# Performance work log

Measured on AMD Instinct MI355X. Metric: run time of the kernel, lower is better.

The kernel has to match this reference:

```python
import jax, jax.numpy as jnp
import numpy as np

A4 = 0.1
EPS = 1e-8  # torch.cosine_similarity eps


def setup_inputs() -> dict:
    key = jax.random.key(0)
    ks = jax.random.split(key, 7)
    N, D, C = 200000, 256, 7
    return {
        "seq": jax.random.normal(ks[0], (N, D), jnp.float32),
        "seq1": jax.random.normal(ks[1], (N, D), jnp.float32),
        "prompt": jax.random.normal(ks[2], (3, D), jnp.float32),
        "w_np": jnp.array([[0.5, 0.4, 0.3]], jnp.float32),  # weighted_prompt init
        "w_ds": jax.random.normal(ks[4], (1, D), jnp.float32) * 0.05,  # downstreamprompt weight
        "w_df": jnp.array([[0.0, 1.0]], jnp.float32),  # weighted_feature init
        "ave": jax.random.normal(ks[6], (C, D), jnp.float32),  # class prototypes (train=0)
    }


def reference(seq, seq1, prompt, w_np, w_ds, w_df, ave):
    # weighted_prompt -> ELU -> 1 + .
    weight = 1.0 + jax.nn.elu(w_np @ prompt)          # [1, D]
    rawret1 = weight * seq                             # [N, D]
    rawret2 = w_ds * seq                               # downstreamprompt
    rawret3 = jax.nn.elu(w_df[0, 0] * rawret1 + w_df[0, 1] * rawret2)
    rawret = rawret3 + A4 * seq1                       # [N, D]
    # per-row cosine similarity vs each class prototype, then softmax
    dots = rawret @ ave.T                              # [N, C]
    nr = jnp.linalg.norm(rawret, axis=1, keepdims=True)   # [N, 1]
    na = jnp.linalg.norm(ave, axis=1)                     # [C]
    sims = dots / jnp.maximum(nr * na[None, :], EPS)
    return jax.nn.softmax(sims, axis=1)
```

## Files before the change

### kernel.cpp

```cpp
#include <hip/hip_runtime.h>
#include <math.h>


__device__ __forceinline__ float elu1(float x) {
    return x > 0.0f ? x : __expf(x) - 1.0f;
}

__device__ __forceinline__ float wave_sum(float v) {
#pragma unroll
    for (int off = 32; off > 0; off >>= 1)
        v += __shfl_xor(v, off, 64);
    return v;
}

__global__ __launch_bounds__(256) void downprompt_kernel(
    const float* __restrict__ seq,
    const float* __restrict__ seq1,
    const float* __restrict__ prompt,
    const float* __restrict__ w_np,
    const float* __restrict__ w_ds,
    const float* __restrict__ w_df,
    const float* __restrict__ ave,
    float* __restrict__ out,
    int N)
{
    const int lane = threadIdx.x & 63;
    const int wavesPerBlock = blockDim.x >> 6;
    const int gwave = blockIdx.x * wavesPerBlock + (threadIdx.x >> 6);
    const int nwave = gridDim.x * wavesPerBlock;
    const int d0 = lane << 2;

    const float a  = w_df[0];
    const float b  = w_df[1];
    const float w0 = w_np[0], w1 = w_np[1], w2 = w_np[2];

    const float4 p0 = *(const float4*)(prompt +   0 + d0);
    const float4 p1 = *(const float4*)(prompt + 256 + d0);
    const float4 p2 = *(const float4*)(prompt + 512 + d0);
    const float4 wd = *(const float4*)(w_ds + d0);

    float coef[4];
    coef[0] = a * (1.0f + elu1(w0*p0.x + w1*p1.x + w2*p2.x)) + b * wd.x;
    coef[1] = a * (1.0f + elu1(w0*p0.y + w1*p1.y + w2*p2.y)) + b * wd.y;
    coef[2] = a * (1.0f + elu1(w0*p0.z + w1*p1.z + w2*p2.z)) + b * wd.z;
    coef[3] = a * (1.0f + elu1(w0*p0.w + w1*p1.w + w2*p2.w)) + b * wd.w;

    float av[7][4];
    float na[7];
#pragma unroll
    for (int c = 0; c < 7; ++c) {
        const float4 v = *(const float4*)(ave + c * 256 + d0);
        av[c][0] = v.x; av[c][1] = v.y; av[c][2] = v.z; av[c][3] = v.w;
        const float p = v.x*v.x + v.y*v.y + v.z*v.z + v.w*v.w;
        na[c] = sqrtf(wave_sum(p));
    }

    for (int row = gwave; row < N; row += nwave) {
        const float4 s = *(const float4*)(seq  + (size_t)row * 256 + d0);
        const float4 t = *(const float4*)(seq1 + (size_t)row * 256 + d0);

        float r[4];
        r[0] = elu1(coef[0] * s.x) + 0.1f * t.x;
        r[1] = elu1(coef[1] * s.y) + 0.1f * t.y;
        r[2] = elu1(coef[2] * s.z) + 0.1f * t.z;
        r[3] = elu1(coef[3] * s.w) + 0.1f * t.w;

        float acc[8];
#pragma unroll
        for (int c = 0; c < 7; ++c)
            acc[c] = r[0]*av[c][0] + r[1]*av[c][1] + r[2]*av[c][2] + r[3]*av[c][3];
        acc[7] = r[0]*r[0] + r[1]*r[1] + r[2]*r[2] + r[3]*r[3];

#pragma unroll
        for (int off = 32; off > 0; off >>= 1) {
#pragma unroll
            for (int k = 0; k < 8; ++k)
                acc[k] += __shfl_xor(acc[k], off, 64);
        }

        const float nr = sqrtf(acc[7]);
        float sims[7];
        float m = -INFINITY;
#pragma unroll
        for (int c = 0; c < 7; ++c) {
            const float den = fmaxf(nr * na[c], 1e-8f);
            sims[c] = acc[c] * __builtin_amdgcn_rcpf(den);
            m = fmaxf(m, sims[c]);
        }
        float sum = 0.0f, mye = 0.0f;
#pragma unroll
        for (int c = 0; c < 7; ++c) {
            const float e = __expf(sims[c] - m);
            sum += e;
            if (lane == c) mye = e;
        }
        if (lane < 7)
            out[(size_t)row * 7 + lane] = mye * __builtin_amdgcn_rcpf(sum);
    }
}

extern "C" void kernel_launch(void* const* d_in, const int* in_sizes, int n_in,
                              void* d_out, int out_size, void* d_ws, size_t ws_size,
                              hipStream_t stream) {
    const float* seq    = (const float*)d_in[0];
    const float* seq1   = (const float*)d_in[1];
    const float* prompt = (const float*)d_in[2];
    const float* w_np   = (const float*)d_in[3];
    const float* w_ds   = (const float*)d_in[4];
    const float* w_df   = (const float*)d_in[5];
    const float* ave    = (const float*)d_in[6];
    float* out = (float*)d_out;

    const int N = in_sizes[0] / 256;

    downprompt_kernel<<<2048, 256, 0, stream>>>(seq, seq1, prompt, w_np, w_ds,
                                                w_df, ave, out, N);
}
```

Measured before the change: 438.3 us.

## Map eight rows per wave with 8-lane groups and short shuffle reductions

```diff
diff --git a/kernel.cpp b/kernel.cpp
--- a/kernel.cpp
+++ b/kernel.cpp
@@ -2,15 +2,10 @@
 #include <math.h>
 
 
+#define NCLS 7
+
 __device__ __forceinline__ float elu1(float x) {
     return x > 0.0f ? x : __expf(x) - 1.0f;
-}
-
-__device__ __forceinline__ float wave_sum(float v) {
-#pragma unroll
-    for (int off = 32; off > 0; off >>= 1)
-        v += __shfl_xor(v, off, 64);
-    return v;
 }
 
 __global__ __launch_bounds__(256) void downprompt_kernel(
@@ -24,78 +19,95 @@
     float* __restrict__ out,
     int N)
 {
-    const int lane = threadIdx.x & 63;
-    const int wavesPerBlock = blockDim.x >> 6;
-    const int gwave = blockIdx.x * wavesPerBlock + (threadIdx.x >> 6);
-    const int nwave = gridDim.x * wavesPerBlock;
-    const int d0 = lane << 2;
+    __shared__ float s_coef[256];
+    __shared__ float s_rna[NCLS];
 
-    const float a  = w_df[0];
-    const float b  = w_df[1];
-    const float w0 = w_np[0], w1 = w_np[1], w2 = w_np[2];
+    const int tid = threadIdx.x;
 
-    const float4 p0 = *(const float4*)(prompt +   0 + d0);
-    const float4 p1 = *(const float4*)(prompt + 256 + d0);
-    const float4 p2 = *(const float4*)(prompt + 512 + d0);
-    const float4 wd = *(const float4*)(w_ds + d0);
+    {
+        const float a  = w_df[0], b = w_df[1];
+        const float w0 = w_np[0], w1 = w_np[1], w2 = w_np[2];
+        const float pd = w0 * prompt[tid] + w1 * prompt[256 + tid]
+                       + w2 * prompt[512 + tid];
+        s_coef[tid] = a * (1.0f + elu1(pd)) + b * w_ds[tid];
+    }
+    if (tid < NCLS) {
+        const float4* av4 = (const float4*)(ave + tid * 256);
+        float s = 0.0f;
+#pragma unroll
+        for (int i = 0; i < 64; ++i) {
+            const float4 v = av4[i];
+            s += v.x * v.x + v.y * v.y + v.z * v.z + v.w * v.w;
+        }
+        s_rna[tid] = rsqrtf(s);
+    }
+    __syncthreads();
 
-    float coef[4];
-    coef[0] = a * (1.0f + elu1(w0*p0.x + w1*p1.x + w2*p2.x)) + b * wd.x;
-    coef[1] = a * (1.0f + elu1(w0*p0.y + w1*p1.y + w2*p2.y)) + b * wd.y;
-    coef[2] = a * (1.0f + elu1(w0*p0.z + w1*p1.z + w2*p2.z)) + b * wd.z;
-    coef[3] = a * (1.0f + elu1(w0*p0.w + w1*p1.w + w2*p2.w)) + b * wd.w;
+    const int lane = tid & 63;
+    const int r = lane >> 3;
+    const int c = lane & 7;
+    const int wv  = blockIdx.x * (blockDim.x >> 6) + (tid >> 6);
+    const int nwv = gridDim.x * (blockDim.x >> 6);
+    const int ngroups = (N + 7) >> 3;
 
-    float av[7][4];
-    float na[7];
+    float rna[NCLS];
 #pragma unroll
-    for (int c = 0; c < 7; ++c) {
-        const float4 v = *(const float4*)(ave + c * 256 + d0);
-        av[c][0] = v.x; av[c][1] = v.y; av[c][2] = v.z; av[c][3] = v.w;
-        const float p = v.x*v.x + v.y*v.y + v.z*v.z + v.w*v.w;
-        na[c] = sqrtf(wave_sum(p));
-    }
+    for (int k = 0; k < NCLS; ++k) rna[k] = s_rna[k];
 
-    for (int row = gwave; row < N; row += nwave) {
-        const float4 s = *(const float4*)(seq  + (size_t)row * 256 + d0);
-        const float4 t = *(const float4*)(seq1 + (size_t)row * 256 + d0);
-
-        float r[4];
-        r[0] = elu1(coef[0] * s.x) + 0.1f * t.x;
-        r[1] = elu1(coef[1] * s.y) + 0.1f * t.y;
-        r[2] = elu1(coef[2] * s.z) + 0.1f * t.z;
-        r[3] = elu1(coef[3] * s.w) + 0.1f * t.w;
+    for (int g = wv; g < ngroups; g += nwv) {
+        const int rowv = (g << 3) + r;
+        const int row  = rowv < N ? rowv : N - 1;
+        const float* srow = seq  + (size_t)row * 256;
+        const float* trow = seq1 + (size_t)row * 256;
 
         float acc[8];
 #pragma unroll
-        for (int c = 0; c < 7; ++c)
-            acc[c] = r[0]*av[c][0] + r[1]*av[c][1] + r[2]*av[c][2] + r[3]*av[c][3];
-        acc[7] = r[0]*r[0] + r[1]*r[1] + r[2]*r[2] + r[3]*r[3];
+        for (int k = 0; k < 8; ++k) acc[k] = 0.0f;
 
 #pragma unroll
-        for (int off = 32; off > 0; off >>= 1) {
+        for (int k = 0; k < 8; ++k) {
+            const int col = k * 32 + c * 4;
+            const float4 s  = *(const float4*)(srow + col);
+            const float4 t  = *(const float4*)(trow + col);
+            const float4 cf = *(const float4*)(s_coef + col);
+
+            const float x0 = elu1(cf.x * s.x) + 0.1f * t.x;
+            const float x1 = elu1(cf.y * s.y) + 0.1f * t.y;
+            const float x2 = elu1(cf.z * s.z) + 0.1f * t.z;
+            const float x3 = elu1(cf.w * s.w) + 0.1f * t.w;
+
+#pragma unroll
+            for (int cl = 0; cl < NCLS; ++cl) {
+                const float4 av = *(const float4*)(ave + cl * 256 + col);
+                acc[cl] += x0 * av.x + x1 * av.y + x2 * av.z + x3 * av.w;
+            }
+            acc[7] += x0 * x0 + x1 * x1 + x2 * x2 + x3 * x3;
+        }
+
+#pragma unroll
+        for (int off = 1; off < 8; off <<= 1) {
 #pragma unroll
             for (int k = 0; k < 8; ++k)
                 acc[k] += __shfl_xor(acc[k], off, 64);
         }
 
-        const float nr = sqrtf(acc[7]);
-        float sims[7];
+        const float rnr = rsqrtf(fmaxf(acc[7], 1e-30f));
+        float sims[NCLS];
         float m = -INFINITY;
 #pragma unroll
-        for (int c = 0; c < 7; ++c) {
-            const float den = fmaxf(nr * na[c], 1e-8f);
-            sims[c] = acc[c] * __builtin_amdgcn_rcpf(den);
-            m = fmaxf(m, sims[c]);
+        for (int cl = 0; cl < NCLS; ++cl) {
+            sims[cl] = acc[cl] * rna[cl] * rnr;
+            m = fmaxf(m, sims[cl]);
         }
         float sum = 0.0f, mye = 0.0f;
 #pragma unroll
-        for (int c = 0; c < 7; ++c) {
-            const float e = __expf(sims[c] - m);
+        for (int cl = 0; cl < NCLS; ++cl) {
+            const float e = __expf(sims[cl] - m);
             sum += e;
-            if (lane == c) mye = e;
+            if (c == cl) mye = e;
         }
-        if (lane < 7)
-            out[(size_t)row * 7 + lane] = mye * __builtin_amdgcn_rcpf(sum);
+        if (c < NCLS && rowv < N)
+            out[(size_t)rowv * NCLS + c] = mye * __builtin_amdgcn_rcpf(sum);
     }
 }
 
@@ -113,6 +125,6 @@
 
     const int N = in_sizes[0] / 256;
 
-    downprompt_kernel<<<2048, 256, 0, stream>>>(seq, seq1, prompt, w_np, w_ds,
+    downprompt_kernel<<<1563, 256, 0, stream>>>(seq, seq1, prompt, w_np, w_ds,
                                                 w_df, ave, out, N);
 }
```

Result: slower. 494.8 us (+12.9%).
